# Performance work log

Measured on AMD Instinct MI355X. Metric: run time of the kernel, lower is better.

## Reference

```python
import jax, jax.numpy as jnp
import numpy as np

B, S, D, K = 16384, 50, 512, 5  # batch, pred_horizon(=steps), dec_units, components_n
H = S  # time_stamp width equals pred_horizon


def setup_inputs() -> dict:
    key = jax.random.key(0)
    ks = jax.random.split(key, 13)
    sc = 0.05
    f32 = jnp.float32
    return {
        "conditions": jax.random.normal(ks[0], (B, S, 3), f32),
        "state_h": jax.random.normal(ks[1], (B, D), f32),
        "state_c": jax.random.normal(ks[2], (B, D), f32),
        # merger LSTM (input = enc_h[D] ++ cond[3])
        "W_m": jax.random.normal(ks[3], (D + 3, 4 * D), f32) * sc,
        "U_m": jax.random.normal(ks[4], (D, 4 * D), f32) * sc,
        "b_m": jnp.zeros((4 * D,), f32),
        # merger MDN heads packed: [alphas|mus_long|sigmas_long|mus_lat|sigmas_lat|rhos]
        "Wh_m": jax.random.normal(ks[5], (D + H, 6 * K), f32) * sc,
        "bh_m": jnp.zeros((6 * K,), f32),
        # yielder LSTM
        "W_y": jax.random.normal(ks[6], (D + 3, 4 * D), f32) * sc,
        "U_y": jax.random.normal(ks[7], (D, 4 * D), f32) * sc,
        "b_y": jnp.zeros((4 * D,), f32),
        # yielder MDN heads packed: [alphas|mus_long|sigmas_long]
        "Wh_y": jax.random.normal(ks[8], (D + H, 3 * K), f32) * sc,
        "bh_y": jnp.zeros((3 * K,), f32),
    }


def _lstm_step(x, h, c, W, U, b):
    # Keras LSTM gate order: i, f, g(cell), o
    z = x @ W + h @ U + b
    i, f, g, o = jnp.split(z, 4, axis=-1)
    c2 = jax.nn.sigmoid(f) * c + jax.nn.sigmoid(i) * jnp.tanh(g)
    h2 = jax.nn.sigmoid(o) * jnp.tanh(c2)
    return h2, c2


def reference(conditions, state_h, state_c, W_m, U_m, b_m, Wh_m, bh_m,
              W_y, U_y, b_y, Wh_y, bh_y):
    # time_stamp[s] = ones in [:s+1] (lower-triangular)
    time_stamp = jnp.tril(jnp.ones((S, H), conditions.dtype))
    enc_h = state_h  # re-fed every step, [B, D]
    # With teacher_percent=1.0 both merger and yielder step conditions are
    # conditions[:, t, :3] at step t (step 0 also uses t=0).
    conds_t = jnp.transpose(conditions, (1, 0, 2))  # [S, B, 3]

    def step(carry, xs):
        h_m, c_m, h_y, c_y = carry
        cond_t, ts = xs  # [B,3], [H]
        x_in = jnp.concatenate([enc_h, cond_t], axis=-1)  # [B, D+3]
        ts_b = jnp.broadcast_to(ts, (h_m.shape[0], H))
        # merger vehicle
        h_m, c_m = _lstm_step(x_in, h_m, c_m, W_m, U_m, b_m)
        feat_m = jnp.concatenate([h_m, ts_b], axis=-1)  # [B, D+H]
        zm = feat_m @ Wh_m + bh_m
        a, ml, sl, mlt, slt, r = jnp.split(zm, 6, axis=-1)
        pm = jnp.concatenate([jax.nn.softmax(a, axis=-1), ml, jnp.exp(sl),
                              mlt, jnp.exp(slt), jnp.tanh(r)], axis=-1)  # [B,30]
        # yielder vehicle
        h_y, c_y = _lstm_step(x_in, h_y, c_y, W_y, U_y, b_y)
        feat_y = jnp.concatenate([h_y, ts_b], axis=-1)
        zy = feat_y @ Wh_y + bh_y
        ay, mly, sly = jnp.split(zy, 3, axis=-1)
        py = jnp.concatenate([jax.nn.softmax(ay, axis=-1), mly, jnp.exp(sly)], axis=-1)  # [B,15]
        return (h_m, c_m, h_y, c_y), (pm, py)

    carry0 = (state_h, state_c, state_h, state_c)
    _, (param_m, param_y) = jax.lax.scan(step, carry0, (conds_t, time_stamp))
    param_m = jnp.transpose(param_m, (1, 0, 2))  # [B, S, 30]
    param_y = jnp.transpose(param_y, (1, 0, 2))  # [B, S, 15]
    return param_m, param_y
```

## Files before the change

### kernel.cpp

```cpp
#include <hip/hip_runtime.h>

typedef __bf16 bf16;
typedef __attribute__((ext_vector_type(8))) __bf16 bf16x8;
typedef __attribute__((ext_vector_type(4))) __bf16 bf16x4;
typedef __attribute__((ext_vector_type(4))) float f32x4;
typedef __attribute__((ext_vector_type(4))) int i32x4;

#define B_TOT 16384
#define SEQ 50
#define DH 512
#define ZW 2048
#define NT 16

#define MFMA16(a, b, c) __builtin_amdgcn_mfma_f32_16x16x32_bf16(a, b, c, 0, 0, 0)

__device__ __forceinline__ float fsigm(float x) {
    return __fdividef(1.0f, 1.0f + __expf(-x));
}
__device__ __forceinline__ float ftanh(float x) {
    float e = __expf(2.0f * x);
    return 1.0f - __fdividef(2.0f, e + 1.0f);
}

__device__ __forceinline__ void gload16(const bf16* g, void* l) {
    __builtin_amdgcn_global_load_lds(
        (const __attribute__((address_space(1))) unsigned int*)g,
        (__attribute__((address_space(3))) unsigned int*)l, 16, 0, 0);
}


__global__ void init_state(const float* __restrict__ sh,
                           bf16* __restrict__ h0m, bf16* __restrict__ h0y) {
    size_t i = (size_t)blockIdx.x * 256 + threadIdx.x;
    bf16 hb = (bf16)sh[i];
    h0m[i] = hb;
    h0y[i] = hb;
}

__global__ void transpose_c(const float* __restrict__ src,
                            float* __restrict__ dM, float* __restrict__ dY) {
    __shared__ float tile[64][65];
    const int tx = blockIdx.x;
    const int ty = blockIdx.y;
    const int lr = threadIdx.x & 63;
    const int lw = threadIdx.x >> 6;
#pragma unroll
    for (int rr = lw; rr < 64; rr += 4)
        tile[rr][lr] = src[(size_t)(tx * 64 + rr) * DH + ty * 64 + lr];
    __syncthreads();
#pragma unroll
    for (int rr = lw; rr < 64; rr += 4) {
        float v = tile[lr][rr];
        size_t o = (size_t)(ty * 64 + rr) * B_TOT + tx * 64 + lr;
        dM[o] = v;
        dY[o] = v;
    }
}

__device__ __forceinline__ int orig_col(int colp) {
    return ((colp >> 4) & 3) * 512 + ((colp >> 6) << 4) + (colp & 15);
}

__global__ void reorder_weights(const float* __restrict__ Um, const float* __restrict__ Uy,
                                const float* __restrict__ Wm, const float* __restrict__ Wy,
                                bf16* __restrict__ UtM, bf16* __restrict__ UtY,
                                bf16* __restrict__ WtM, bf16* __restrict__ WtY) {
    int idx = blockIdx.x * 256 + threadIdx.x;
    int which = idx >> 20;
    int r = idx & ((1 << 20) - 1);
    int colp = r >> 9, k = r & 511;
    int orig = orig_col(colp);
    const float* src = which == 0 ? Um : which == 1 ? Uy : which == 2 ? Wm : Wy;
    bf16* dst = which == 0 ? UtM : which == 1 ? UtY : which == 2 ? WtM : WtY;
    int cb = colp >> 4, fr = colp & 15;
    int kt = k >> 5, fq = (k >> 3) & 3, e = k & 7;
    int lane = fq * 16 + fr;
    dst[(((size_t)(cb * 16 + kt) * 64 + lane) << 3) + e] = (bf16)src[(size_t)k * ZW + orig];
}

__global__ void build_wc2(const float* __restrict__ Wm, const float* __restrict__ Wy,
                          float* __restrict__ Wc2M, float* __restrict__ Wc2Y) {
    int idx = blockIdx.x * 256 + threadIdx.x;
    if (idx >= 2 * 512 * 12) return;
    int which = idx / 6144;
    int r2 = idx % 6144;
    int hcol = r2 / 12, rg = r2 % 12;
    int r = rg >> 2, g = rg & 3;
    const float* src = which ? Wy : Wm;
    float* dst = which ? Wc2Y : Wc2M;
    dst[hcol * 12 + rg] = src[(size_t)(512 + r) * ZW + g * 512 + hcol];
}

__global__ void cond_transpose(const float* __restrict__ cond, float* __restrict__ condT4) {
    int idx = blockIdx.x * 256 + threadIdx.x;
    if (idx >= SEQ * B_TOT) return;
    int t = idx / B_TOT, row = idx % B_TOT;
    const float* s = cond + ((size_t)row * SEQ + t) * 3;
    f32x4 v = {s[0], s[1], s[2], 0.f};
    *(f32x4*)(condT4 + (size_t)idx * 4) = v;
}

__global__ void build_heads(const float* __restrict__ Whm, const float* __restrict__ bhm,
                            const float* __restrict__ Why, const float* __restrict__ bhy,
                            bf16* __restrict__ WhmT, bf16* __restrict__ WhyT,
                            float* __restrict__ tscm, float* __restrict__ tscy) {
    int i = blockIdx.x * 256 + threadIdx.x;
    const int N1 = 32 * 512, N2 = 16 * 512, N3 = SEQ * 32, N4 = SEQ * 16;
    if (i < N1) {
        int n = i >> 9, k = i & 511;
        WhmT[i] = (bf16)(n < 30 ? Whm[k * 30 + n] : 0.f);
    } else if (i < N1 + N2) {
        int j = i - N1;
        int n = j >> 9, k = j & 511;
        WhyT[j] = (bf16)(n < 15 ? Why[k * 15 + n] : 0.f);
    } else if (i < N1 + N2 + N3) {
        int j = i - (N1 + N2);
        int tt = j >> 5, col = j & 31;
        float v = 0.f;
        if (col < 30) {
            v = bhm[col];
            for (int s = 0; s <= tt; ++s) v += Whm[(512 + s) * 30 + col];
        }
        tscm[j] = v;
    } else if (i < N1 + N2 + N3 + N4) {
        int j = i - (N1 + N2 + N3);
        int tt = j >> 4, col = j & 15;
        float v = 0.f;
        if (col < 15) {
            v = bhy[col];
            for (int s = 0; s <= tt; ++s) v += Why[(512 + s) * 15 + col];
        }
        tscy[j] = v;
    }
}


#define FENCE() asm volatile("" ::: "memory")
#define BARRIER()                        \
    do {                                 \
        FENCE();                         \
        __builtin_amdgcn_s_barrier();    \
        FENCE();                         \
    } while (0)
#define WAIT_LGKM0()                                          \
    do {                                                      \
        asm volatile("s_waitcnt lgkmcnt(0)" ::: "memory");    \
        __builtin_amdgcn_sched_barrier(0);                    \
    } while (0)
#define WAIT_VM(n)                                                  \
    do {                                                            \
        asm volatile("s_waitcnt vmcnt(" #n ")" ::: "memory");       \
        __builtin_amdgcn_sched_barrier(0);                          \
    } while (0)

template <int MODE>
__global__ __launch_bounds__(256, 4) void gemm_step(
    const bf16* __restrict__ Am, const bf16* __restrict__ Ay,
    const bf16* __restrict__ BtM, const bf16* __restrict__ BtY,
    const bf16* __restrict__ xwM, const bf16* __restrict__ xwY,
    const float* __restrict__ Wc2M, const float* __restrict__ Wc2Y,
    const float* __restrict__ biasM, const float* __restrict__ biasY,
    float* __restrict__ cM, float* __restrict__ cY,
    bf16* __restrict__ hoM, bf16* __restrict__ hoY,
    bf16* __restrict__ xoM, bf16* __restrict__ xoY,
    const float* __restrict__ condT4, int t) {
    __shared__ bf16 As[3][128][32];

    const int tid = threadIdx.x;
    const int wave = tid >> 6, lane = tid & 63;
    const int lin = blockIdx.y * 128 + blockIdx.x;
    const int xcd = lin & 7, jj = lin >> 3;
    const int bx = xcd * 16 + (jj >> 4);
    const int by = jj & 15;
    const int brow = bx * 128;
    const int bz = blockIdx.z;
    const bf16* A = bz ? Ay : Am;
    const bf16* Bt = bz ? BtY : BtM;

    const int fr = lane & 15, fq = lane >> 4;
    const int wr = wave >> 1, wc = wave & 1;

    const int srow = tid >> 2;
    const int sc8 = (((tid & 3) ^ ((srow >> 1) & 3)) << 3);
    const bf16* Asrc = A + (size_t)(brow + srow) * DH + sc8;
    char* stA = (char*)As + wave * 1024;

    const int cxor = ((fq ^ ((fr >> 1) & 3)) << 4);
    const char* Ard = (char*)As + (wr * 64 + fr) * 64 + cxor;

    const uint64_t bbase =
        (uint64_t)(const char*)Bt + (uint64_t)(by * 8 + wc * 4) * 16384 + lane * 16;

    f32x4 acc[4][4];
#pragma unroll
    for (int m = 0; m < 4; ++m)
#pragma unroll
        for (int n = 0; n < 4; ++n) acc[m][n] = (f32x4){0.f, 0.f, 0.f, 0.f};

    i32x4 bgbuf[2][4];

#define STAGE(slot, kts)                                    \
    do {                                                    \
        const bf16* _s = Asrc + (kts) * 32;                 \
        char* _d = stA + (slot) * 8192;                     \
        gload16(_s, _d);                                    \
        gload16(_s + 64 * DH, _d + 4096);                   \
    } while (0)

#define BGLOAD(bank, kts)                                                        \
    do {                                                                         \
        uint64_t _a = bbase + (uint64_t)(kts) * 1024;                            \
        asm volatile("global_load_dwordx4 %0, %1, off"                          \
                     : "=&v"(bgbuf[bank][0]) : "v"(_a) : "memory");              \
        asm volatile("global_load_dwordx4 %0, %1, off"                          \
                     : "=&v"(bgbuf[bank][1]) : "v"(_a + 16384) : "memory");      \
        asm volatile("global_load_dwordx4 %0, %1, off"                          \
                     : "=&v"(bgbuf[bank][2]) : "v"(_a + 32768) : "memory");      \
        asm volatile("global_load_dwordx4 %0, %1, off"                          \
                     : "=&v"(bgbuf[bank][3]) : "v"(_a + 49152) : "memory");      \
    } while (0)

    BGLOAD(0, 0);
    STAGE(0, 0);
    STAGE(1, 1);
    WAIT_VM(2);
    BARRIER();

#pragma unroll
    for (int kt = 0; kt < NT - 1; ++kt) {
        const int rcur = kt % 3;
        STAGE((kt + 2) % 3, (kt + 2 < NT) ? kt + 2 : NT - 1);
        BGLOAD((kt + 1) & 1, kt + 1);
        bf16x8 af[4];
        {
            const char* _a = Ard + rcur * 8192;
            af[0] = *(const bf16x8*)(_a);
            af[1] = *(const bf16x8*)(_a + 1024);
            af[2] = *(const bf16x8*)(_a + 2048);
            af[3] = *(const bf16x8*)(_a + 3072);
        }
        WAIT_LGKM0();
        WAIT_VM(6);
        __builtin_amdgcn_s_setprio(1);
#pragma unroll
        for (int m = 0; m < 4; ++m)
#pragma unroll
            for (int n = 0; n < 4; ++n)
                acc[m][n] = MFMA16(af[m], __builtin_bit_cast(bf16x8, bgbuf[kt & 1][n]),
                                   acc[m][n]);
        __builtin_amdgcn_s_setprio(0);
        __builtin_amdgcn_sched_barrier(0);
        BARRIER();
    }
    {
        bf16x8 af[4];
        const char* _a = Ard + ((NT - 1) % 3) * 8192;
        af[0] = *(const bf16x8*)(_a);
        af[1] = *(const bf16x8*)(_a + 1024);
        af[2] = *(const bf16x8*)(_a + 2048);
        af[3] = *(const bf16x8*)(_a + 3072);
        WAIT_LGKM0();
        WAIT_VM(0);
        __builtin_amdgcn_s_setprio(1);
#pragma unroll
        for (int m = 0; m < 4; ++m)
#pragma unroll
            for (int n = 0; n < 4; ++n)
                acc[m][n] = MFMA16(af[m], __builtin_bit_cast(bf16x8, bgbuf[(NT - 1) & 1][n]),
                                   acc[m][n]);
        __builtin_amdgcn_s_setprio(0);
        __builtin_amdgcn_sched_barrier(0);
    }

    const int jb = by * 2 + wc;
    const int hcol = jb * 16 + fr;
    const int rowbase = brow + wr * 64 + fq * 4;

    if (MODE == 0) {
        const float* bias = bz ? biasY : biasM;
        bf16* XO = bz ? xoY : xoM;
        float b0 = bias[hcol], b1 = bias[512 + hcol], b2 = bias[1024 + hcol],
              b3 = bias[1536 + hcol];
#pragma unroll
        for (int m = 0; m < 4; ++m) {
            const int row0 = rowbase + m * 16;
            bf16x8 v0, v1;
#pragma unroll
            for (int j = 0; j < 2; ++j) {
                v0[j * 4 + 0] = (bf16)(acc[m][0][j] + b0);
                v0[j * 4 + 1] = (bf16)(acc[m][1][j] + b1);
                v0[j * 4 + 2] = (bf16)(acc[m][2][j] + b2);
                v0[j * 4 + 3] = (bf16)(acc[m][3][j] + b3);
            }
#pragma unroll
            for (int j = 2; j < 4; ++j) {
                v1[(j - 2) * 4 + 0] = (bf16)(acc[m][0][j] + b0);
                v1[(j - 2) * 4 + 1] = (bf16)(acc[m][1][j] + b1);
                v1[(j - 2) * 4 + 2] = (bf16)(acc[m][2][j] + b2);
                v1[(j - 2) * 4 + 3] = (bf16)(acc[m][3][j] + b3);
            }
            bf16* o = XO + ((size_t)hcol * B_TOT + row0) * 4;
            *(bf16x8*)(o) = v0;
            *(bf16x8*)(o + 8) = v1;
        }
    } else {
        float* Cb = bz ? cY : cM;
        bf16* Ho = bz ? hoY : hoM;
        const bf16* xw = bz ? xwY : xwM;
        const float* Wc2 = bz ? Wc2Y : Wc2M;
        f32x4 wcv0 = *(const f32x4*)(Wc2 + hcol * 12);
        f32x4 wcv1 = *(const f32x4*)(Wc2 + hcol * 12 + 4);
        f32x4 wcv2 = *(const f32x4*)(Wc2 + hcol * 12 + 8);
#pragma unroll
        for (int m = 0; m < 4; ++m) {
            const int row0 = rowbase + m * 16;
            const bf16* xp = xw + ((size_t)hcol * B_TOT + row0) * 4;
            bf16x8 xv0 = *(const bf16x8*)(xp);
            bf16x8 xv1 = *(const bf16x8*)(xp + 8);
            f32x4 cvm = *(const f32x4*)(Cb + (size_t)hcol * B_TOT + row0);
            f32x4 cd[4];
#pragma unroll
            for (int j = 0; j < 4; ++j)
                cd[j] = *(const f32x4*)(condT4 + ((size_t)t * B_TOT + row0 + j) * 4);
            f32x4 cnew;
#pragma unroll
            for (int j = 0; j < 4; ++j) {
                float z[4];
#pragma unroll
                for (int g = 0; g < 4; ++g) {
                    float xwv = (j < 2) ? (float)xv0[j * 4 + g] : (float)xv1[(j - 2) * 4 + g];
                    z[g] = acc[m][g][j] + xwv + cd[j][0] * wcv0[g] + cd[j][1] * wcv1[g] +
                           cd[j][2] * wcv2[g];
                }
                float ii = fsigm(z[0]);
                float ff = fsigm(z[1]);
                float gg = ftanh(z[2]);
                float oo = fsigm(z[3]);
                float cn = ff * cvm[j] + ii * gg;
                cnew[j] = cn;
                Ho[(size_t)(row0 + j) * DH + hcol] = (bf16)(oo * ftanh(cn));
            }
            *(f32x4*)(Cb + (size_t)hcol * B_TOT + row0) = cnew;
        }
    }
#undef STAGE
#undef BGLOAD
}

__global__ __launch_bounds__(128) void heads_step(
    const bf16* __restrict__ hm, const bf16* __restrict__ hy,
    const bf16* __restrict__ WhmT, const bf16* __restrict__ WhyT,
    const float* __restrict__ tscm, const float* __restrict__ tscy,
    float* __restrict__ out, int t) {
    __shared__ float zbuf[2 * 768];
    const int tid = threadIdx.x, wave = tid >> 6, lane = tid & 63;
    const int fr = lane & 15, fq = lane >> 4;
    const int rbase = blockIdx.x * 32 + wave * 16;

    f32x4 am0 = {0.f, 0.f, 0.f, 0.f}, am1 = {0.f, 0.f, 0.f, 0.f}, ay0 = {0.f, 0.f, 0.f, 0.f};

    for (int k0 = 0; k0 < DH; k0 += 32) {
        const size_t ao = (size_t)(rbase + fr) * DH + k0 + fq * 8;
        bf16x8 a0 = *(const bf16x8*)(hm + ao);
        bf16x8 y0 = *(const bf16x8*)(hy + ao);
        const size_t bo = (size_t)fr * DH + k0 + fq * 8;
        bf16x8 b0 = *(const bf16x8*)(WhmT + bo);
        bf16x8 b1 = *(const bf16x8*)(WhmT + bo + 16 * DH);
        bf16x8 yb = *(const bf16x8*)(WhyT + bo);
        am0 = MFMA16(a0, b0, am0);
        am1 = MFMA16(a0, b1, am1);
        ay0 = MFMA16(y0, yb, ay0);
    }

    float* zm = zbuf + wave * 768;
    float* zy = zm + 512;
#pragma unroll
    for (int j = 0; j < 4; ++j) {
        int rl = fq * 4 + j;
        zm[rl * 32 + fr] = am0[j] + tscm[t * 32 + fr];
        zm[rl * 32 + 16 + fr] = am1[j] + tscm[t * 32 + 16 + fr];
        zy[rl * 16 + fr] = ay0[j] + tscy[t * 16 + fr];
    }
    __syncthreads();

    const int r = lane & 15;
    const size_t grow = (size_t)rbase + r;
    if (lane < 16) {
        float z[30];
#pragma unroll
        for (int i = 0; i < 30; ++i) z[i] = zm[r * 32 + i];
        float* o = out + (grow * SEQ + t) * 30;
        float mx = z[0];
#pragma unroll
        for (int i = 1; i < 5; ++i) mx = fmaxf(mx, z[i]);
        float e[5], s = 0.f;
#pragma unroll
        for (int i = 0; i < 5; ++i) {
            e[i] = __expf(z[i] - mx);
            s += e[i];
        }
        float inv = __fdividef(1.f, s);
#pragma unroll
        for (int i = 0; i < 5; ++i) o[i] = e[i] * inv;
#pragma unroll
        for (int i = 5; i < 10; ++i) o[i] = z[i];
#pragma unroll
        for (int i = 10; i < 15; ++i) o[i] = __expf(z[i]);
#pragma unroll
        for (int i = 15; i < 20; ++i) o[i] = z[i];
#pragma unroll
        for (int i = 20; i < 25; ++i) o[i] = __expf(z[i]);
#pragma unroll
        for (int i = 25; i < 30; ++i) o[i] = ftanh(z[i]);
    } else if (lane < 32) {
        float z[15];
#pragma unroll
        for (int i = 0; i < 15; ++i) z[i] = zy[r * 16 + i];
        float* o = out + (size_t)B_TOT * SEQ * 30 + (grow * SEQ + t) * 15;
        float mx = z[0];
#pragma unroll
        for (int i = 1; i < 5; ++i) mx = fmaxf(mx, z[i]);
        float e[5], s = 0.f;
#pragma unroll
        for (int i = 0; i < 5; ++i) {
            e[i] = __expf(z[i] - mx);
            s += e[i];
        }
        float inv = __fdividef(1.f, s);
#pragma unroll
        for (int i = 0; i < 5; ++i) o[i] = e[i] * inv;
#pragma unroll
        for (int i = 5; i < 10; ++i) o[i] = z[i];
#pragma unroll
        for (int i = 10; i < 15; ++i) o[i] = __expf(z[i]);
    }
}

extern "C" void kernel_launch(void* const* d_in, const int* in_sizes, int n_in,
                              void* d_out, int out_size, void* d_ws, size_t ws_size,
                              hipStream_t stream) {
    const float* cond = (const float*)d_in[0];
    const float* sh = (const float*)d_in[1];
    const float* sc = (const float*)d_in[2];
    const float* Wm = (const float*)d_in[3];
    const float* Um = (const float*)d_in[4];
    const float* bm = (const float*)d_in[5];
    const float* Whm = (const float*)d_in[6];
    const float* bhm = (const float*)d_in[7];
    const float* Wy = (const float*)d_in[8];
    const float* Uy = (const float*)d_in[9];
    const float* by_ = (const float*)d_in[10];
    const float* Why = (const float*)d_in[11];
    const float* bhy = (const float*)d_in[12];
    float* out = (float*)d_out;

    char* p = (char*)d_ws;
    auto take = [&](size_t bytes) {
        char* r = p;
        p += (bytes + 255) & ~(size_t)255;
        return r;
    };
    bf16* UtM = (bf16*)take((size_t)ZW * DH * 2);
    bf16* UtY = (bf16*)take((size_t)ZW * DH * 2);
    bf16* WtM = (bf16*)take((size_t)ZW * DH * 2);
    bf16* WtY = (bf16*)take((size_t)ZW * DH * 2);
    float* Wc2M = (float*)take(512 * 12 * 4);
    float* Wc2Y = (float*)take(512 * 12 * 4);
    bf16* WhmT = (bf16*)take(32 * DH * 2);
    bf16* WhyT = (bf16*)take(16 * DH * 2);
    float* tscm = (float*)take(SEQ * 32 * 4);
    float* tscy = (float*)take(SEQ * 16 * 4);
    float* condT4 = (float*)take((size_t)SEQ * B_TOT * 4 * 4);
    bf16* xwM = (bf16*)take((size_t)B_TOT * ZW * 2);
    bf16* xwY = (bf16*)take((size_t)B_TOT * ZW * 2);
    bf16* hM0 = (bf16*)take((size_t)B_TOT * DH * 2);
    bf16* hM1 = (bf16*)take((size_t)B_TOT * DH * 2);
    bf16* hY0 = (bf16*)take((size_t)B_TOT * DH * 2);
    bf16* hY1 = (bf16*)take((size_t)B_TOT * DH * 2);
    float* cMb = (float*)take((size_t)B_TOT * DH * 4);
    float* cYb = (float*)take((size_t)B_TOT * DH * 4);
    bf16* hM[2] = {hM0, hM1};
    bf16* hY[2] = {hY0, hY1};

    init_state<<<(B_TOT * DH) / 256, 256, 0, stream>>>(sh, hM0, hY0);
    transpose_c<<<dim3(B_TOT / 64, DH / 64), 256, 0, stream>>>(sc, cMb, cYb);
    reorder_weights<<<(4 * ZW * DH) / 256, 256, 0, stream>>>(Um, Uy, Wm, Wy, UtM, UtY, WtM, WtY);
    build_wc2<<<(2 * 512 * 12 + 255) / 256, 256, 0, stream>>>(Wm, Wy, Wc2M, Wc2Y);
    cond_transpose<<<(SEQ * B_TOT + 255) / 256, 256, 0, stream>>>(cond, condT4);
    build_heads<<<(32 * 512 + 16 * 512 + SEQ * 32 + SEQ * 16 + 255) / 256, 256, 0, stream>>>(
        Whm, bhm, Why, bhy, WhmT, WhyT, tscm, tscy);

    dim3 ggrid(B_TOT / 128, ZW / 128, 2);
    gemm_step<0><<<ggrid, 256, 0, stream>>>(hM0, hM0, WtM, WtY, nullptr, nullptr,
                                            nullptr, nullptr, bm, by_, nullptr, nullptr,
                                            nullptr, nullptr, xwM, xwY, condT4, 0);

    for (int t = 0; t < SEQ; ++t) {
        const int a = t & 1, b = (t + 1) & 1;
        gemm_step<1><<<ggrid, 256, 0, stream>>>(hM[a], hY[a], UtM, UtY, xwM, xwY,
                                                Wc2M, Wc2Y, nullptr, nullptr, cMb, cYb,
                                                hM[b], hY[b], nullptr, nullptr, condT4, t);
        heads_step<<<B_TOT / 32, 128, 0, stream>>>(hM[b], hY[b], WhmT, WhyT, tscm, tscy, out, t);
    }
}
```

Measured before the change: 8.001 ms.

## Store hidden state in MFMA fragment layout and load A directly to registers

The hidden state h is now written in a pre-swizzled MFMA-fragment layout, so the recurrent GEMM can load A operands straight from global memory into registers, the same way it loads B. This removes the LDS staging, swizzle, and per-k-tile barriers. The cell state and xW buffers are moved to a row-group-major layout to match, and the heads kernel reads the new h layout. It trades LDS reuse across waves for more global and L2 traffic plus higher register pressure, and lowers launch_bounds occupancy from 4 to 3.

```diff
diff --git a/kernel.cpp b/kernel.cpp
--- a/kernel.cpp
+++ b/kernel.cpp
@@ -22,39 +22,26 @@
     return 1.0f - __fdividef(2.0f, e + 1.0f);
 }
 
-__device__ __forceinline__ void gload16(const bf16* g, void* l) {
-    __builtin_amdgcn_global_load_lds(
-        (const __attribute__((address_space(1))) unsigned int*)g,
-        (__attribute__((address_space(3))) unsigned int*)l, 16, 0, 0);
-}
-
 
 __global__ void init_state(const float* __restrict__ sh,
                            bf16* __restrict__ h0m, bf16* __restrict__ h0y) {
     size_t i = (size_t)blockIdx.x * 256 + threadIdx.x;
+    int row = i >> 9, k = i & 511;
+    size_t off = (((size_t)(row >> 4) * 16 + (k >> 5)) * 64 + ((k >> 3) & 3) * 16 +
+                  (row & 15)) * 8 + (k & 7);
     bf16 hb = (bf16)sh[i];
-    h0m[i] = hb;
-    h0y[i] = hb;
-}
-
-__global__ void transpose_c(const float* __restrict__ src,
-                            float* __restrict__ dM, float* __restrict__ dY) {
-    __shared__ float tile[64][65];
-    const int tx = blockIdx.x;
-    const int ty = blockIdx.y;
-    const int lr = threadIdx.x & 63;
-    const int lw = threadIdx.x >> 6;
-#pragma unroll
-    for (int rr = lw; rr < 64; rr += 4)
-        tile[rr][lr] = src[(size_t)(tx * 64 + rr) * DH + ty * 64 + lr];
-    __syncthreads();
-#pragma unroll
-    for (int rr = lw; rr < 64; rr += 4) {
-        float v = tile[lr][rr];
-        size_t o = (size_t)(ty * 64 + rr) * B_TOT + tx * 64 + lr;
-        dM[o] = v;
-        dY[o] = v;
-    }
+    h0m[off] = hb;
+    h0y[off] = hb;
+}
+
+__global__ void build_c3(const float* __restrict__ src,
+                         float* __restrict__ dM, float* __restrict__ dY) {
+    size_t i = (size_t)blockIdx.x * 256 + threadIdx.x;
+    int row = i >> 9, hcol = i & 511;
+    float v = src[i];
+    size_t o = ((size_t)(row >> 2) * 512 + hcol) * 4 + (row & 3);
+    dM[o] = v;
+    dY[o] = v;
 }
 
 __device__ __forceinline__ int orig_col(int colp) {
@@ -135,18 +122,6 @@
 }
 
 
-#define FENCE() asm volatile("" ::: "memory")
-#define BARRIER()                        \
-    do {                                 \
-        FENCE();                         \
-        __builtin_amdgcn_s_barrier();    \
-        FENCE();                         \
-    } while (0)
-#define WAIT_LGKM0()                                          \
-    do {                                                      \
-        asm volatile("s_waitcnt lgkmcnt(0)" ::: "memory");    \
-        __builtin_amdgcn_sched_barrier(0);                    \
-    } while (0)
 #define WAIT_VM(n)                                                  \
     do {                                                            \
         asm volatile("s_waitcnt vmcnt(" #n ")" ::: "memory");       \
@@ -154,7 +129,7 @@
     } while (0)
 
 template <int MODE>
-__global__ __launch_bounds__(256, 4) void gemm_step(
+__global__ __launch_bounds__(256, 3) void gemm_step(
     const bf16* __restrict__ Am, const bf16* __restrict__ Ay,
     const bf16* __restrict__ BtM, const bf16* __restrict__ BtY,
     const bf16* __restrict__ xwM, const bf16* __restrict__ xwY,
@@ -164,14 +139,12 @@
     bf16* __restrict__ hoM, bf16* __restrict__ hoY,
     bf16* __restrict__ xoM, bf16* __restrict__ xoY,
     const float* __restrict__ condT4, int t) {
-    __shared__ bf16 As[3][128][32];
-
     const int tid = threadIdx.x;
     const int wave = tid >> 6, lane = tid & 63;
     const int lin = blockIdx.y * 128 + blockIdx.x;
-    const int xcd = lin & 7, jj = lin >> 3;
-    const int bx = xcd * 16 + (jj >> 4);
-    const int by = jj & 15;
+    const int xcd = lin & 7, jj2 = lin >> 3;
+    const int bx = xcd * 16 + (jj2 >> 4);
+    const int by = jj2 & 15;
     const int brow = bx * 128;
     const int bz = blockIdx.z;
     const bf16* A = bz ? Ay : Am;
@@ -180,14 +153,8 @@
     const int fr = lane & 15, fq = lane >> 4;
     const int wr = wave >> 1, wc = wave & 1;
 
-    const int srow = tid >> 2;
-    const int sc8 = (((tid & 3) ^ ((srow >> 1) & 3)) << 3);
-    const bf16* Asrc = A + (size_t)(brow + srow) * DH + sc8;
-    char* stA = (char*)As + wave * 1024;
-
-    const int cxor = ((fq ^ ((fr >> 1) & 3)) << 4);
-    const char* Ard = (char*)As + (wr * 64 + fr) * 64 + cxor;
-
+    const uint64_t abase =
+        (uint64_t)(const char*)A + (uint64_t)(bx * 8 + wr * 4) * 16384 + lane * 16;
     const uint64_t bbase =
         (uint64_t)(const char*)Bt + (uint64_t)(by * 8 + wc * 4) * 16384 + lane * 16;
 
@@ -197,84 +164,66 @@
 #pragma unroll
         for (int n = 0; n < 4; ++n) acc[m][n] = (f32x4){0.f, 0.f, 0.f, 0.f};
 
-    i32x4 bgbuf[2][4];
-
-#define STAGE(slot, kts)                                    \
-    do {                                                    \
-        const bf16* _s = Asrc + (kts) * 32;                 \
-        char* _d = stA + (slot) * 8192;                     \
-        gload16(_s, _d);                                    \
-        gload16(_s + 64 * DH, _d + 4096);                   \
+    i32x4 afr[2][4], bfr[2][4];
+
+#define AGLOAD(bank, kts)                                                         \
+    do {                                                                          \
+        uint64_t _a = abase + (uint64_t)(kts) * 1024;                             \
+        asm volatile("global_load_dwordx4 %0, %1, off"                            \
+                     : "=&v"(afr[bank][0]) : "v"(_a) : "memory");                 \
+        asm volatile("global_load_dwordx4 %0, %1, off"                            \
+                     : "=&v"(afr[bank][1]) : "v"(_a + 16384) : "memory");         \
+        asm volatile("global_load_dwordx4 %0, %1, off"                            \
+                     : "=&v"(afr[bank][2]) : "v"(_a + 32768) : "memory");         \
+        asm volatile("global_load_dwordx4 %0, %1, off"                            \
+                     : "=&v"(afr[bank][3]) : "v"(_a + 49152) : "memory");         \
     } while (0)
-
-#define BGLOAD(bank, kts)                                                        \
-    do {                                                                         \
-        uint64_t _a = bbase + (uint64_t)(kts) * 1024;                            \
-        asm volatile("global_load_dwordx4 %0, %1, off"                          \
-                     : "=&v"(bgbuf[bank][0]) : "v"(_a) : "memory");              \
-        asm volatile("global_load_dwordx4 %0, %1, off"                          \
-                     : "=&v"(bgbuf[bank][1]) : "v"(_a + 16384) : "memory");      \
-        asm volatile("global_load_dwordx4 %0, %1, off"                          \
-                     : "=&v"(bgbuf[bank][2]) : "v"(_a + 32768) : "memory");      \
-        asm volatile("global_load_dwordx4 %0, %1, off"                          \
-                     : "=&v"(bgbuf[bank][3]) : "v"(_a + 49152) : "memory");      \
+#define BGLOAD(bank, kts)                                                         \
+    do {                                                                          \
+        uint64_t _b = bbase + (uint64_t)(kts) * 1024;                             \
+        asm volatile("global_load_dwordx4 %0, %1, off"                            \
+                     : "=&v"(bfr[bank][0]) : "v"(_b) : "memory");                 \
+        asm volatile("global_load_dwordx4 %0, %1, off"                            \
+                     : "=&v"(bfr[bank][1]) : "v"(_b + 16384) : "memory");         \
+        asm volatile("global_load_dwordx4 %0, %1, off"                            \
+                     : "=&v"(bfr[bank][2]) : "v"(_b + 32768) : "memory");         \
+        asm volatile("global_load_dwordx4 %0, %1, off"                            \
+                     : "=&v"(bfr[bank][3]) : "v"(_b + 49152) : "memory");         \
     } while (0)
 
+    AGLOAD(0, 0);
     BGLOAD(0, 0);
-    STAGE(0, 0);
-    STAGE(1, 1);
-    WAIT_VM(2);
-    BARRIER();
-
-#pragma unroll
-    for (int kt = 0; kt < NT - 1; ++kt) {
-        const int rcur = kt % 3;
-        STAGE((kt + 2) % 3, (kt + 2 < NT) ? kt + 2 : NT - 1);
-        BGLOAD((kt + 1) & 1, kt + 1);
-        bf16x8 af[4];
-        {
-            const char* _a = Ard + rcur * 8192;
-            af[0] = *(const bf16x8*)(_a);
-            af[1] = *(const bf16x8*)(_a + 1024);
-            af[2] = *(const bf16x8*)(_a + 2048);
-            af[3] = *(const bf16x8*)(_a + 3072);
-        }
-        WAIT_LGKM0();
-        WAIT_VM(6);
+    AGLOAD(1, 1);
+    BGLOAD(1, 1);
+
+#pragma unroll
+    for (int kt = 0; kt < NT; ++kt) {
+        if (kt < NT - 1) {
+            WAIT_VM(8);
+        } else {
+            WAIT_VM(0);
+        }
         __builtin_amdgcn_s_setprio(1);
 #pragma unroll
         for (int m = 0; m < 4; ++m)
 #pragma unroll
             for (int n = 0; n < 4; ++n)
-                acc[m][n] = MFMA16(af[m], __builtin_bit_cast(bf16x8, bgbuf[kt & 1][n]),
-                                   acc[m][n]);
+                acc[m][n] = MFMA16(__builtin_bit_cast(bf16x8, afr[kt & 1][m]),
+                                   __builtin_bit_cast(bf16x8, bfr[kt & 1][n]), acc[m][n]);
         __builtin_amdgcn_s_setprio(0);
         __builtin_amdgcn_sched_barrier(0);
-        BARRIER();
-    }
-    {
-        bf16x8 af[4];
-        const char* _a = Ard + ((NT - 1) % 3) * 8192;
-        af[0] = *(const bf16x8*)(_a);
-        af[1] = *(const bf16x8*)(_a + 1024);
-        af[2] = *(const bf16x8*)(_a + 2048);
-        af[3] = *(const bf16x8*)(_a + 3072);
-        WAIT_LGKM0();
-        WAIT_VM(0);
-        __builtin_amdgcn_s_setprio(1);
-#pragma unroll
-        for (int m = 0; m < 4; ++m)
-#pragma unroll
-            for (int n = 0; n < 4; ++n)
-                acc[m][n] = MFMA16(af[m], __builtin_bit_cast(bf16x8, bgbuf[(NT - 1) & 1][n]),
-                                   acc[m][n]);
-        __builtin_amdgcn_s_setprio(0);
-        __builtin_amdgcn_sched_barrier(0);
-    }
+        if (kt + 2 < NT) {
+            AGLOAD(kt & 1, kt + 2);
+            BGLOAD(kt & 1, kt + 2);
+        }
+    }
+#undef AGLOAD
+#undef BGLOAD
 
     const int jb = by * 2 + wc;
     const int hcol = jb * 16 + fr;
     const int rowbase = brow + wr * 64 + fq * 4;
+    const int rb0 = (rowbase >> 2);
 
     if (MODE == 0) {
         const float* bias = bz ? biasY : biasM;
@@ -283,7 +232,6 @@
               b3 = bias[1536 + hcol];
 #pragma unroll
         for (int m = 0; m < 4; ++m) {
-            const int row0 = rowbase + m * 16;
             bf16x8 v0, v1;
 #pragma unroll
             for (int j = 0; j < 2; ++j) {
@@ -299,7 +247,7 @@
                 v1[(j - 2) * 4 + 2] = (bf16)(acc[m][2][j] + b2);
                 v1[(j - 2) * 4 + 3] = (bf16)(acc[m][3][j] + b3);
             }
-            bf16* o = XO + ((size_t)hcol * B_TOT + row0) * 4;
+            bf16* o = XO + ((size_t)(rb0 + m * 4) * 512 + hcol) * 16;
             *(bf16x8*)(o) = v0;
             *(bf16x8*)(o + 8) = v1;
         }
@@ -311,18 +259,24 @@
         f32x4 wcv0 = *(const f32x4*)(Wc2 + hcol * 12);
         f32x4 wcv1 = *(const f32x4*)(Wc2 + hcol * 12 + 4);
         f32x4 wcv2 = *(const f32x4*)(Wc2 + hcol * 12 + 8);
+        const int ktc = jb >> 1;
+        const int fqp = (jb & 1) * 2 + (fr >> 3);
+        bf16* hob = Ho + (((size_t)((brow >> 4) + wr * 4) * 16 + ktc) * 64 + fqp * 16 +
+                          fq * 4) * 8 + (fr & 7);
 #pragma unroll
         for (int m = 0; m < 4; ++m) {
-            const int row0 = rowbase + m * 16;
-            const bf16* xp = xw + ((size_t)hcol * B_TOT + row0) * 4;
+            const size_t co = ((size_t)(rb0 + m * 4) * 512 + hcol);
+            const bf16* xp = xw + co * 16;
             bf16x8 xv0 = *(const bf16x8*)(xp);
             bf16x8 xv1 = *(const bf16x8*)(xp + 8);
-            f32x4 cvm = *(const f32x4*)(Cb + (size_t)hcol * B_TOT + row0);
+            f32x4 cvm = *(const f32x4*)(Cb + co * 4);
+            const int row0 = rowbase + m * 16;
             f32x4 cd[4];
 #pragma unroll
             for (int j = 0; j < 4; ++j)
                 cd[j] = *(const f32x4*)(condT4 + ((size_t)t * B_TOT + row0 + j) * 4);
             f32x4 cnew;
+            bf16* hom = hob + (size_t)m * 16 * 64 * 8;
 #pragma unroll
             for (int j = 0; j < 4; ++j) {
                 float z[4];
@@ -338,13 +292,11 @@
                 float oo = fsigm(z[3]);
                 float cn = ff * cvm[j] + ii * gg;
                 cnew[j] = cn;
-                Ho[(size_t)(row0 + j) * DH + hcol] = (bf16)(oo * ftanh(cn));
+                hom[j * 8] = (bf16)(oo * ftanh(cn));
             }
-            *(f32x4*)(Cb + (size_t)hcol * B_TOT + row0) = cnew;
-        }
-    }
-#undef STAGE
-#undef BGLOAD
+            *(f32x4*)(Cb + co * 4) = cnew;
+        }
+    }
 }
 
 __global__ __launch_bounds__(128) void heads_step(
@@ -356,13 +308,15 @@
     const int tid = threadIdx.x, wave = tid >> 6, lane = tid & 63;
     const int fr = lane & 15, fq = lane >> 4;
     const int rbase = blockIdx.x * 32 + wave * 16;
+    const int rg = rbase >> 4;
 
     f32x4 am0 = {0.f, 0.f, 0.f, 0.f}, am1 = {0.f, 0.f, 0.f, 0.f}, ay0 = {0.f, 0.f, 0.f, 0.f};
 
-    for (int k0 = 0; k0 < DH; k0 += 32) {
-        const size_t ao = (size_t)(rbase + fr) * DH + k0 + fq * 8;
+    for (int kt = 0; kt < 16; ++kt) {
+        const size_t ao = ((size_t)(rg * 16 + kt) * 64 + lane) * 8;
         bf16x8 a0 = *(const bf16x8*)(hm + ao);
         bf16x8 y0 = *(const bf16x8*)(hy + ao);
+        const int k0 = kt * 32;
         const size_t bo = (size_t)fr * DH + k0 + fq * 8;
         bf16x8 b0 = *(const bf16x8*)(WhmT + bo);
         bf16x8 b1 = *(const bf16x8*)(WhmT + bo + 16 * DH);
@@ -483,7 +437,7 @@
     bf16* hY[2] = {hY0, hY1};
 
     init_state<<<(B_TOT * DH) / 256, 256, 0, stream>>>(sh, hM0, hY0);
-    transpose_c<<<dim3(B_TOT / 64, DH / 64), 256, 0, stream>>>(sc, cMb, cYb);
+    build_c3<<<(B_TOT * DH) / 256, 256, 0, stream>>>(sc, cMb, cYb);
     reorder_weights<<<(4 * ZW * DH) / 256, 256, 0, stream>>>(Um, Uy, Wm, Wy, UtM, UtY, WtM, WtY);
     build_wc2<<<(2 * 512 * 12 + 255) / 256, 256, 0, stream>>>(Wm, Wy, Wc2M, Wc2Y);
     cond_transpose<<<(SEQ * B_TOT + 255) / 256, 256, 0, stream>>>(cond, condT4);
```

Measured after the change: 7.164 ms. 10.5% less time.
